# Optimization experiments

Measured on AMD Instinct MI355X. Metric: run time of the kernel, lower is better.

The kernel has to match this reference:

```python
import jax, jax.numpy as jnp
import numpy as np

N_NODES = 50000
N_EDGES = 600000
N_GRAPHS = 128
EMB = 128
LAYERS = 5
BN_EPS = 1e-5


def setup_inputs() -> dict:
    key = jax.random.key(0)
    ks = jax.random.split(key, 16)
    inp = {}
    inp['batch'] = jnp.sort(jax.random.randint(ks[0], (N_NODES,), 0, N_GRAPHS)).astype(jnp.int64 if jax.config.jax_enable_x64 else jnp.int32)
    inp['x'] = jax.random.normal(ks[1], (N_NODES, 48), dtype=jnp.float32)
    inp['edge_index'] = jax.random.randint(ks[2], (2, N_EDGES), 0, N_NODES)
    inp['edge_attr'] = jax.random.normal(ks[3], (N_EDGES, 11), dtype=jnp.float32)
    inp['edge_weight'] = jnp.ones((N_EDGES,), dtype=jnp.float32)
    # parameters (xavier-ish scaling)
    inp['W_atom'] = jax.random.normal(ks[4], (48, EMB), dtype=jnp.float32) * (1.0 / np.sqrt(48))
    inp['b_atom'] = jnp.zeros((EMB,), dtype=jnp.float32)
    inp['W_bond'] = jax.random.normal(ks[5], (11, EMB), dtype=jnp.float32) * (1.0 / np.sqrt(11))
    inp['b_bond'] = jnp.zeros((EMB,), dtype=jnp.float32)
    inp['Wl'] = jax.random.normal(ks[6], (LAYERS, EMB, EMB), dtype=jnp.float32) * (1.0 / np.sqrt(EMB))
    inp['bl'] = jnp.zeros((LAYERS, EMB), dtype=jnp.float32)
    inp['Wr'] = jax.random.normal(ks[7], (LAYERS, EMB, EMB), dtype=jnp.float32) * (1.0 / np.sqrt(EMB))
    inp['gamma'] = jnp.ones((LAYERS, EMB), dtype=jnp.float32)
    inp['beta'] = jnp.zeros((LAYERS, EMB), dtype=jnp.float32)
    return inp


def reference(batch, x, edge_index, edge_attr, edge_weight,
              W_atom, b_atom, W_bond, b_bond, Wl, bl, Wr, gamma, beta):
    src = edge_index[0]
    dst = edge_index[1]
    # encoders
    h = x @ W_atom + b_atom                      # [N, EMB]
    ea = edge_attr @ W_bond + b_bond             # [E, EMB]
    # mean-aggregation denominator (in-degree, count-based)
    deg = jax.ops.segment_sum(jnp.ones_like(edge_weight), dst, num_segments=N_NODES)
    denom = jnp.maximum(deg, 1.0)[:, None]       # [N, 1]
    xs = []
    for i in range(LAYERS):
        # SAGEConv: mean over (x_j + edge_attr) * w_e, then lin_l(agg) + lin_r(x)
        msg = (h[src] + ea) * edge_weight[:, None]          # [E, EMB]
        agg = jax.ops.segment_sum(msg, dst, num_segments=N_NODES) / denom
        h = agg @ Wl[i] + bl[i] + h @ Wr[i]
        # BatchNorm1d (training: batch statistics, biased variance)
        mu = jnp.mean(h, axis=0)
        var = jnp.var(h, axis=0)
        h = gamma[i] * (h - mu) * jax.lax.rsqrt(var + BN_EPS) + beta[i]
        if i < LAYERS - 1:
            h = jax.nn.relu(h)
        # dropout with drop_ratio=0.0 is identity
        xs.append(h)
    # layerwise global_add_pool + concat
    xpool = jnp.concatenate(
        [jax.ops.segment_sum(xi, batch, num_segments=N_GRAPHS) for xi in xs], axis=1)
    return (xpool, h)
```

## Files before the change

kernel.cpp:

```cpp
#include <hip/hip_runtime.h>
#include <hip/hip_bf16.h>

#define NNODES 50000
#define NEDGES 600000
#define NGRAPHS 128
#define EMB 128
#define NLAYERS 5
#define BN_EPS 1e-5f
#define STATW 8
#define SCAN_BLOCKS ((NNODES + 255) / 256)
#define NSB ((NNODES + 255) / 256)
#define EAB ((NNODES + 31) / 32)
#define BPB ((NLAYERS * 32768 + 255) / 256)

typedef short s16x8 __attribute__((ext_vector_type(8)));
typedef float f32x16 __attribute__((ext_vector_type(16)));

__device__ __forceinline__ short f2bf(float f) {
    unsigned u = __builtin_bit_cast(unsigned, f);
    unsigned r = (u + 0x7fffu + ((u >> 16) & 1u)) >> 16;
    return (short)r;
}
__device__ __forceinline__ float bf2f(short s) {
    return __builtin_bit_cast(float, ((unsigned)(unsigned short)s) << 16);
}

__device__ __forceinline__ float2 stat_sum(const float* __restrict__ st, int t) {
    float s = 0.f, q = 0.f;
#pragma unroll
    for (int k = 0; k < STATW; k++) {
        s += st[k * 256 + t];
        q += st[k * 256 + 128 + t];
    }
    return make_float2(s, q);
}

__global__ __launch_bounds__(256) void init_kernel(int* __restrict__ deg,
                                                   float* __restrict__ stat) {
    int i = blockIdx.x * 256 + threadIdx.x;
    if (i < NNODES) deg[i] = 0;
    if (i < NLAYERS * STATW * 256) stat[i] = 0.f;
}

__global__ __launch_bounds__(256) void deg_kernel(const int* __restrict__ ei,
                                                  int* __restrict__ deg,
                                                  int* __restrict__ rank) {
    int e = blockIdx.x * 256 + threadIdx.x;
    if (e >= NEDGES) return;
    rank[e] = atomicAdd(&deg[ei[NEDGES + e]], 1);
}

__global__ __launch_bounds__(256) void scan1(const int* __restrict__ deg,
                                             int* __restrict__ local_excl,
                                             int* __restrict__ part) {
    __shared__ int sh[256];
    int t = threadIdx.x;
    int i = blockIdx.x * 256 + t;
    int v = (i < NNODES) ? deg[i] : 0;
    sh[t] = v;
    __syncthreads();
    for (int off = 1; off < 256; off <<= 1) {
        int u = (t >= off) ? sh[t - off] : 0;
        __syncthreads();
        sh[t] += u;
        __syncthreads();
    }
    if (i < NNODES) local_excl[i] = sh[t] - v;
    if (t == 255) part[blockIdx.x] = sh[255];
}

__global__ __launch_bounds__(256) void scan23(const int* __restrict__ part,
                                              const int* __restrict__ local_excl,
                                              int* __restrict__ rowptr) {
    __shared__ int sh[256];
    int t = threadIdx.x;
    int v = (t < SCAN_BLOCKS) ? part[t] : 0;
    sh[t] = v;
    __syncthreads();
    for (int off = 1; off < 256; off <<= 1) {
        int u = (t >= off) ? sh[t - off] : 0;
        __syncthreads();
        sh[t] += u;
        __syncthreads();
    }
    int bo = (blockIdx.x == 0) ? 0 : sh[blockIdx.x - 1];
    int i = blockIdx.x * 256 + t;
    if (i < NNODES) rowptr[i] = local_excl[i] + bo;
    if (blockIdx.x == 0 && t == 0) rowptr[NNODES] = sh[SCAN_BLOCKS - 1];
}

__global__ __launch_bounds__(256) void edge_fill(const int* __restrict__ ei,
                                                 const float* __restrict__ ew,
                                                 const float* __restrict__ eattr,
                                                 const int* __restrict__ rowptr,
                                                 const int* __restrict__ rank,
                                                 int* __restrict__ epk) {
    int e = blockIdx.x * 256 + threadIdx.x;
    if (e >= NEDGES) return;
    int src = ei[e];
    int dst = ei[NEDGES + e];
    int pos = rowptr[dst] + rank[e];
    int pk[8];
    pk[0] = src;
    pk[1] = __float_as_int(ew[e]);
    unsigned short a[12];
#pragma unroll
    for (int j = 0; j < 11; j++) a[j] = (unsigned short)f2bf(eattr[e * 11 + j]);
    a[11] = 0;
#pragma unroll
    for (int j = 0; j < 6; j++)
        pk[2 + j] = (int)a[2 * j] | ((int)a[2 * j + 1] << 16);
    int* dstp = epk + (size_t)pos * 8;
    *(int4*)dstp = *(int4*)pk;
    *(int4*)(dstp + 4) = *(int4*)(pk + 4);
}

__global__ __launch_bounds__(256) void prep2(const int* __restrict__ rowptr,
                                             const int* __restrict__ epk,
                                             int2* __restrict__ epg,
                                             const float* __restrict__ Wb,
                                             const float* __restrict__ bbond,
                                             short* __restrict__ Ehi,
                                             const float* __restrict__ X,
                                             const float* __restrict__ Wa,
                                             const float* __restrict__ ba,
                                             short* __restrict__ Hhi,
                                             const float* __restrict__ Wl,
                                             const float* __restrict__ Wr,
                                             short* __restrict__ Bf) {
    __shared__ float shpool[1792];
    int blk = blockIdx.x;
    int t = threadIdx.x;

    if (blk < NSB) {
        float* Wb_s = shpool;
        float* bb_s = shpool + 1408;
        for (int i = t; i < 1408; i += 256) Wb_s[i] = Wb[i];
        if (t < 128) bb_s[t] = bbond[t];
        __syncthreads();
        int node = blk * 256 + t;
        if (node >= NNODES) return;
        int b = rowptr[node], e = rowptr[node + 1];
        float s[11];
#pragma unroll
        for (int j = 0; j < 11; j++) s[j] = 0.f;
        float ws = 0.f;
        for (int p = b; p < e; p++) {
            const int* pk = epk + (size_t)p * 8;
            int4 lo = *(const int4*)pk;
            int4 hi = *(const int4*)(pk + 4);
            float w = __int_as_float(lo.y);
            ws += w;
            epg[p] = make_int2(lo.x, lo.y);
            int packed[6] = {lo.z, lo.w, hi.x, hi.y, hi.z, hi.w};
#pragma unroll
            for (int j = 0; j < 11; j++) {
                short v = (short)((packed[j >> 1] >> ((j & 1) * 16)) & 0xffff);
                s[j] += bf2f(v) * w;
            }
        }
        short* erow = Ehi + (size_t)node * 128;
#pragma unroll
        for (int c8 = 0; c8 < 16; c8++) {
            s16x8 o;
#pragma unroll
            for (int jj = 0; jj < 8; jj++) {
                int c = c8 * 8 + jj;
                float a = bb_s[c] * ws;
#pragma unroll
                for (int j = 0; j < 11; j++) a += s[j] * Wb_s[j * 128 + c];
                o[jj] = f2bf(a);
            }
            *(s16x8*)(erow + c8 * 8) = o;
        }
    } else if (blk < NSB + EAB) {
        float* as = shpool;
        int row0 = (blk - NSB) * 32;
        for (int i = t; i < 32 * 48; i += 256) {
            int r = i / 48, k = i - r * 48;
            int gr = row0 + r;
            as[k * 36 + r] = (gr < NNODES) ? X[gr * 48 + k] : 0.f;
        }
        __syncthreads();
        int c = t & 127, rh = t >> 7;
        float acc[16];
#pragma unroll
        for (int i = 0; i < 16; i++) acc[i] = 0.f;
        for (int k = 0; k < 48; k++) {
            float w = Wa[k * 128 + c];
            const float* rowv = &as[k * 36 + rh * 16];
            float4 v0 = *(const float4*)(rowv + 0);
            float4 v1 = *(const float4*)(rowv + 4);
            float4 v2 = *(const float4*)(rowv + 8);
            float4 v3 = *(const float4*)(rowv + 12);
            acc[0] += v0.x * w;  acc[1] += v0.y * w;
            acc[2] += v0.z * w;  acc[3] += v0.w * w;
            acc[4] += v1.x * w;  acc[5] += v1.y * w;
            acc[6] += v1.z * w;  acc[7] += v1.w * w;
            acc[8] += v2.x * w;  acc[9] += v2.y * w;
            acc[10] += v2.z * w; acc[11] += v2.w * w;
            acc[12] += v3.x * w; acc[13] += v3.y * w;
            acc[14] += v3.z * w; acc[15] += v3.w * w;
        }
        float bb = ba[c];
        for (int i = 0; i < 16; i++) {
            int gr = row0 + rh * 16 + i;
            if (gr < NNODES) Hhi[(size_t)gr * 128 + c] = f2bf(acc[i] + bb);
        }
    } else {
        int idx = (blk - NSB - EAB) * 256 + t;
        if (idx >= NLAYERS * 32768) return;
        int layer = idx >> 15;
        int r = idx & 32767;
        int k = r >> 7, col = r & 127;
        float w = (k < 128) ? Wl[layer * 16384 + k * 128 + col]
                            : Wr[layer * 16384 + (k - 128) * 128 + col];
        short hi = f2bf(w);
        short lo = f2bf(w - bf2f(hi));
        int ks = k >> 4, half = (k >> 3) & 1, j = k & 7;
        int nt = col >> 5, n32 = col & 31;
        int fo = ((nt * 2 + half) * 32 + n32) * 8 + j;
        short* base = Bf + (size_t)layer * 65536 + ks * 4096;
        base[fo] = hi;
        base[2048 + fo] = lo;
    }
}

__global__ __launch_bounds__(256) void agg_kernel(const short* __restrict__ Hsrc,
                                                  const short* __restrict__ Ehi,
                                                  const int* __restrict__ rowptr,
                                                  const int2* __restrict__ epg,
                                                  const float* __restrict__ stat,
                                                  const float* __restrict__ gamma,
                                                  const float* __restrict__ beta,
                                                  short* __restrict__ Ahi) {
    __shared__ float cscs[128], cshs[128];
    int t = threadIdx.x;
    if (t < 128) {
        float sc = 1.f, sh = 0.f;
        if (stat) {
            const float invM = 1.f / (float)NNODES;
            float2 sq = stat_sum(stat, t);
            float mu = sq.x * invM;
            float var = sq.y * invM - mu * mu;
            sc = gamma[t] * rsqrtf(var + BN_EPS);
            sh = beta[t] - mu * sc;
        }
        cscs[t] = sc;
        cshs[t] = sh;
    }
    __syncthreads();
    int lane = t & 15, grp = t >> 4;
    int c8 = lane * 8;
    int node = blockIdx.x * 16 + grp;
    if (node >= NNODES) return;
    float rlo = stat ? 0.f : -3.4e38f;
    float sc[8], sh[8];
#pragma unroll
    for (int j = 0; j < 8; j++) { sc[j] = cscs[c8 + j]; sh[j] = cshs[c8 + j]; }
    int b = rowptr[node], e = rowptr[node + 1];
    float s[8];
#pragma unroll
    for (int j = 0; j < 8; j++) s[j] = 0.f;
    int p = b;
    for (; p + 3 < e; p += 4) {
        int2 e0 = epg[p], e1 = epg[p + 1], e2 = epg[p + 2], e3 = epg[p + 3];
        float w0 = __int_as_float(e0.y), w1 = __int_as_float(e1.y);
        float w2 = __int_as_float(e2.y), w3 = __int_as_float(e3.y);
        s16x8 h0 = *(const s16x8*)&Hsrc[(size_t)e0.x * 128 + c8];
        s16x8 h1 = *(const s16x8*)&Hsrc[(size_t)e1.x * 128 + c8];
        s16x8 h2 = *(const s16x8*)&Hsrc[(size_t)e2.x * 128 + c8];
        s16x8 h3 = *(const s16x8*)&Hsrc[(size_t)e3.x * 128 + c8];
#pragma unroll
        for (int j = 0; j < 8; j++) {
            float v0 = fmaxf(bf2f(h0[j]) * sc[j] + sh[j], rlo);
            float v1 = fmaxf(bf2f(h1[j]) * sc[j] + sh[j], rlo);
            float v2 = fmaxf(bf2f(h2[j]) * sc[j] + sh[j], rlo);
            float v3 = fmaxf(bf2f(h3[j]) * sc[j] + sh[j], rlo);
            s[j] += v0 * w0 + v1 * w1 + v2 * w2 + v3 * w3;
        }
    }
    for (; p < e; p++) {
        int2 pk0 = epg[p];
        float w0 = __int_as_float(pk0.y);
        s16x8 h0 = *(const s16x8*)&Hsrc[(size_t)pk0.x * 128 + c8];
#pragma unroll
        for (int j = 0; j < 8; j++)
            s[j] += fmaxf(bf2f(h0[j]) * sc[j] + sh[j], rlo) * w0;
    }
    float inv = 1.f / fmaxf((float)(e - b), 1.f);
    s16x8 ea = *(const s16x8*)&Ehi[(size_t)node * 128 + c8];
    s16x8 o;
#pragma unroll
    for (int j = 0; j < 8; j++) o[j] = f2bf((s[j] + bf2f(ea[j])) * inv);
    *(s16x8*)&Ahi[(size_t)node * 128 + c8] = o;
}

__global__ __launch_bounds__(256) void layer_gemm(const short* __restrict__ Ahi,
                                                  const short* __restrict__ Hsrc,
                                                  const float* __restrict__ statp,
                                                  const float* __restrict__ gamma,
                                                  const float* __restrict__ beta,
                                                  const short* __restrict__ Bf,
                                                  const float* __restrict__ bias,
                                                  short* __restrict__ Cbf,
                                                  float* __restrict__ stat) {
    __shared__ float s_s[128], s_q[128];
    __shared__ float csc[128], csh[128];
    int t = threadIdx.x;
    int wave = t >> 6, lane = t & 63;
    int n32 = lane & 31, half = lane >> 5;
    int row0 = blockIdx.x * 128 + wave * 32;

    if (t < 128) {
        s_s[t] = 0.f;
        s_q[t] = 0.f;
        float sc = 1.f, sh = 0.f;
        if (statp) {
            const float invM = 1.f / (float)NNODES;
            float2 sq = stat_sum(statp, t);
            float mu = sq.x * invM;
            float var = sq.y * invM - mu * mu;
            sc = gamma[t] * rsqrtf(var + BN_EPS);
            sh = beta[t] - mu * sc;
        }
        csc[t] = sc;
        csh[t] = sh;
    }
    __syncthreads();
    float rlo = statp ? 0.f : -3.4e38f;

    int myrow = row0 + n32;
    bool rowok = myrow < NNODES;
    size_t rbase = (size_t)myrow * 128;
    int acol = half * 8;

    f32x16 acc[4];
#pragma unroll
    for (int i = 0; i < 4; i++) acc[i] = (f32x16)(0.f);

    const short* bb0 = Bf + half * 256 + n32 * 8;

    s16x8 ahA = {0, 0, 0, 0, 0, 0, 0, 0}, ahB = {0, 0, 0, 0, 0, 0, 0, 0};
    s16x8 bhA[4], blA[4], bhB[4], blB[4];
    if (rowok) {
        ahA = *(const s16x8*)(Ahi + rbase + acol);
        ahB = *(const s16x8*)(Ahi + rbase + 16 + acol);
    }
#pragma unroll
    for (int nt = 0; nt < 4; nt++) {
        bhA[nt] = *(const s16x8*)(bb0 + nt * 512);
        blA[nt] = *(const s16x8*)(bb0 + 2048 + nt * 512);
        bhB[nt] = *(const s16x8*)(bb0 + 4096 + nt * 512);
        blB[nt] = *(const s16x8*)(bb0 + 4096 + 2048 + nt * 512);
    }

#pragma unroll
    for (int ks = 0; ks < 16; ks++) {
        s16x8 ahC = {0, 0, 0, 0, 0, 0, 0, 0};
        s16x8 bhC[4], blC[4];
        if (ks < 14) {
            int kn = ks + 2;
            if (rowok) {
                if (kn < 8) {
                    ahC = *(const s16x8*)(Ahi + rbase + kn * 16 + acol);
                } else {
                    s16x8 hv = *(const s16x8*)(Hsrc + rbase + (kn & 7) * 16 + acol);
                    int kc = (kn & 7) * 16 + acol;
#pragma unroll
                    for (int j = 0; j < 8; j++)
                        ahC[j] = f2bf(fmaxf(bf2f(hv[j]) * csc[kc + j] +
                                            csh[kc + j], rlo));
                }
            }
            const short* bbn = bb0 + kn * 4096;
#pragma unroll
            for (int nt = 0; nt < 4; nt++) {
                bhC[nt] = *(const s16x8*)(bbn + nt * 512);
                blC[nt] = *(const s16x8*)(bbn + 2048 + nt * 512);
            }
        }
#pragma unroll
        for (int nt = 0; nt < 4; nt++) {
            acc[nt] = __builtin_amdgcn_mfma_f32_32x32x16_bf16(ahA, bhA[nt], acc[nt], 0, 0, 0);
            acc[nt] = __builtin_amdgcn_mfma_f32_32x32x16_bf16(ahA, blA[nt], acc[nt], 0, 0, 0);
        }
        ahA = ahB;
        ahB = ahC;
#pragma unroll
        for (int nt = 0; nt < 4; nt++) {
            bhA[nt] = bhB[nt];
            blA[nt] = blB[nt];
            bhB[nt] = bhC[nt];
            blB[nt] = blC[nt];
        }
    }

#pragma unroll
    for (int nt = 0; nt < 4; nt++) {
        int col = nt * 32 + n32;
        float bb = bias[col];
        float ss = 0.f, qq = 0.f;
#pragma unroll
        for (int reg = 0; reg < 16; reg++) {
            int r = row0 + (reg & 3) + 8 * (reg >> 2) + 4 * half;
            if (r < NNODES) {
                float v = acc[nt][reg] + bb;
                Cbf[(size_t)r * 128 + col] = f2bf(v);
                ss += v;
                qq += v * v;
            }
        }
        ss += __shfl_xor(ss, 32);
        qq += __shfl_xor(qq, 32);
        if (half == 0) {
            atomicAdd(&s_s[col], ss);
            atomicAdd(&s_q[col], qq);
        }
    }
    __syncthreads();
    if (t < 128) {
        int slot = blockIdx.x & (STATW - 1);
        atomicAdd(&stat[slot * 256 + t], s_s[t]);
        atomicAdd(&stat[slot * 256 + 128 + t], s_q[t]);
    }
}

__global__ __launch_bounds__(256) void pool5(const short* __restrict__ Cbf,
                                             const float* __restrict__ stat,
                                             const float* __restrict__ gamma,
                                             const float* __restrict__ beta,
                                             const int* __restrict__ batch,
                                             float* __restrict__ pool,
                                             float* __restrict__ Hf32) {
    __shared__ float csc[128], csh[128];
    __shared__ float sred[8][128];
    __shared__ int srange[2];
    int t = threadIdx.x;
    int u = blockIdx.x;
    int g = u / NLAYERS, l = u - g * NLAYERS;
    if (t < 2) {
        int target = g + t;
        int lo = 0, hi = NNODES;
        while (lo < hi) {
            int mid = (lo + hi) >> 1;
            if (batch[mid] < target) lo = mid + 1; else hi = mid;
        }
        srange[t] = lo;
    }
    if (t < 128) {
        const float invM = 1.f / (float)NNODES;
        float2 sq = stat_sum(stat + l * STATW * 256, t);
        float mu = sq.x * invM;
        float var = sq.y * invM - mu * mu;
        float sc = gamma[l * 128 + t] * rsqrtf(var + BN_EPS);
        csc[t] = sc;
        csh[t] = beta[l * 128 + t] - mu * sc;
    }
    __syncthreads();
    int gstart = srange[0], gend = srange[1];
    int lane = t & 31, grp = t >> 5;
    int c4 = lane * 4;
    float4 sc = *(const float4*)&csc[c4];
    float4 sh = *(const float4*)&csh[c4];
    const short* Cl = Cbf + (size_t)l * NNODES * 128;
    float4 accp = make_float4(0.f, 0.f, 0.f, 0.f);
    int relu = (l < NLAYERS - 1);
    for (int r = gstart + grp; r < gend; r += 8) {
        ushort4 cv = *(const ushort4*)&Cl[(size_t)r * 128 + c4];
        float4 v;
        v.x = bf2f((short)cv.x) * sc.x + sh.x;
        v.y = bf2f((short)cv.y) * sc.y + sh.y;
        v.z = bf2f((short)cv.z) * sc.z + sh.z;
        v.w = bf2f((short)cv.w) * sc.w + sh.w;
        if (relu) {
            v.x = fmaxf(v.x, 0.f);
            v.y = fmaxf(v.y, 0.f);
            v.z = fmaxf(v.z, 0.f);
            v.w = fmaxf(v.w, 0.f);
        } else {
            *(float4*)&Hf32[(size_t)r * 128 + c4] = v;
        }
        accp.x += v.x;
        accp.y += v.y;
        accp.z += v.z;
        accp.w += v.w;
    }
    sred[grp][c4 + 0] = accp.x;
    sred[grp][c4 + 1] = accp.y;
    sred[grp][c4 + 2] = accp.z;
    sred[grp][c4 + 3] = accp.w;
    __syncthreads();
    if (t < 128) {
        float s = 0.f;
#pragma unroll
        for (int k = 0; k < 8; k++) s += sred[k][t];
        pool[(size_t)g * 640 + l * 128 + t] = s;
    }
}

extern "C" void kernel_launch(void* const* d_in, const int* in_sizes, int n_in,
                              void* d_out, int out_size, void* d_ws, size_t ws_size,
                              hipStream_t stream) {
    const int* batch = (const int*)d_in[0];
    const float* x = (const float*)d_in[1];
    const int* edge_index = (const int*)d_in[2];
    const float* edge_attr = (const float*)d_in[3];
    const float* edge_weight = (const float*)d_in[4];
    const float* W_atom = (const float*)d_in[5];
    const float* b_atom = (const float*)d_in[6];
    const float* W_bond = (const float*)d_in[7];
    const float* b_bond = (const float*)d_in[8];
    const float* Wl = (const float*)d_in[9];
    const float* bl = (const float*)d_in[10];
    const float* Wr = (const float*)d_in[11];
    const float* gamma = (const float*)d_in[12];
    const float* beta = (const float*)d_in[13];
    float* out = (float*)d_out;

    char* ws = (char*)d_ws;
    size_t off = 0;
    auto alloc = [&](size_t bytes) -> void* {
        void* p = ws + off;
        off += (bytes + 255) & ~(size_t)255;
        return p;
    };
    short* Hhi = (short*)alloc((size_t)NNODES * 128 * 2);
    short* Ahi = (short*)alloc((size_t)NNODES * 128 * 2);
    short* Ehi = (short*)alloc((size_t)NNODES * 128 * 2);
    short* Cbf = (short*)alloc((size_t)NLAYERS * NNODES * 128 * 2);
    int* epk = (int*)alloc((size_t)NEDGES * 32);
    int2* epg = (int2*)alloc((size_t)NEDGES * 8);
    int* rank = (int*)alloc((size_t)NEDGES * 4);
    int* rowptr = (int*)alloc((size_t)(NNODES + 1) * 4);
    int* deg = (int*)alloc((size_t)NNODES * 4);
    float* stat = (float*)alloc(NLAYERS * STATW * 256 * 4);
    int* local_excl = (int*)alloc((size_t)NNODES * 4);
    int* part = (int*)alloc(SCAN_BLOCKS * 4);
    short* Bf = (short*)alloc((size_t)NLAYERS * 65536 * 2);

    init_kernel<<<SCAN_BLOCKS, 256, 0, stream>>>(deg, stat);
    deg_kernel<<<(NEDGES + 255) / 256, 256, 0, stream>>>(edge_index, deg, rank);
    scan1<<<SCAN_BLOCKS, 256, 0, stream>>>(deg, local_excl, part);
    scan23<<<SCAN_BLOCKS, 256, 0, stream>>>(part, local_excl, rowptr);
    edge_fill<<<(NEDGES + 255) / 256, 256, 0, stream>>>(edge_index, edge_weight,
                                                        edge_attr, rowptr, rank, epk);
    prep2<<<NSB + EAB + BPB, 256, 0, stream>>>(rowptr, epk, epg, W_bond, b_bond, Ehi,
                                               x, W_atom, b_atom, Hhi, Wl, Wr, Bf);

    const short* src = Hhi;
    for (int i = 0; i < NLAYERS; i++) {
        const float* st = (i == 0) ? nullptr : stat + (size_t)(i - 1) * STATW * 256;
        const float* gm = (i == 0) ? nullptr : gamma + (i - 1) * 128;
        const float* bt = (i == 0) ? nullptr : beta + (i - 1) * 128;
        short* Ci = Cbf + (size_t)i * NNODES * 128;
        agg_kernel<<<(NNODES + 15) / 16, 256, 0, stream>>>(src, Ehi, rowptr, epg,
                                                           st, gm, bt, Ahi);
        layer_gemm<<<(NNODES + 127) / 128, 256, 0, stream>>>(
            Ahi, src, st, gm, bt, Bf + (size_t)i * 65536, bl + i * 128, Ci,
            stat + (size_t)i * STATW * 256);
        src = Ci;
    }

    pool5<<<NGRAPHS * NLAYERS, 256, 0, stream>>>(
        Cbf, stat, gamma, beta, batch, out, out + (size_t)NGRAPHS * 640);
}
```

Before: 491.2 us.

## Split edge-encoder nodes across 8 lanes and use MFMA for atom encoder

```diff
diff --git a/kernel.cpp b/kernel.cpp
--- a/kernel.cpp
+++ b/kernel.cpp
@@ -9,9 +9,9 @@
 #define BN_EPS 1e-5f
 #define STATW 8
 #define SCAN_BLOCKS ((NNODES + 255) / 256)
-#define NSB ((NNODES + 255) / 256)
-#define EAB ((NNODES + 31) / 32)
-#define BPB ((NLAYERS * 32768 + 255) / 256)
+#define NSB2 ((NNODES + 31) / 32)
+#define EAMB ((NNODES + 127) / 128)
+#define BPB2 ((NLAYERS * 32768 + 255) / 256)
 
 typedef short s16x8 __attribute__((ext_vector_type(8)));
 typedef float f32x16 __attribute__((ext_vector_type(16)));
@@ -36,10 +36,23 @@
 }
 
 __global__ __launch_bounds__(256) void init_kernel(int* __restrict__ deg,
-                                                   float* __restrict__ stat) {
+                                                   float* __restrict__ stat,
+                                                   const float* __restrict__ Wa,
+                                                   short* __restrict__ Waf) {
     int i = blockIdx.x * 256 + threadIdx.x;
     if (i < NNODES) deg[i] = 0;
     if (i < NLAYERS * STATW * 256) stat[i] = 0.f;
+    if (i < 48 * 128) {
+        int k = i >> 7, col = i & 127;
+        float w = Wa[k * 128 + col];
+        short hi = f2bf(w);
+        short lo = f2bf(w - bf2f(hi));
+        int ks = k >> 4, half = (k >> 3) & 1, j = k & 7;
+        int nt = col >> 5, n32 = col & 31;
+        int fo = ((nt * 2 + half) * 32 + n32) * 8 + j;
+        Waf[ks * 4096 + fo] = hi;
+        Waf[ks * 4096 + 2048 + fo] = lo;
+    }
 }
 
 __global__ __launch_bounds__(256) void deg_kernel(const int* __restrict__ ei,
@@ -122,93 +135,111 @@
                                              const float* __restrict__ bbond,
                                              short* __restrict__ Ehi,
                                              const float* __restrict__ X,
-                                             const float* __restrict__ Wa,
                                              const float* __restrict__ ba,
                                              short* __restrict__ Hhi,
                                              const float* __restrict__ Wl,
                                              const float* __restrict__ Wr,
-                                             short* __restrict__ Bf) {
-    __shared__ float shpool[1792];
+                                             short* __restrict__ Bf,
+                                             const short* __restrict__ Waf) {
+    __shared__ float shpool[1536];
     int blk = blockIdx.x;
     int t = threadIdx.x;
 
-    if (blk < NSB) {
+    if (blk < NSB2) {
         float* Wb_s = shpool;
         float* bb_s = shpool + 1408;
         for (int i = t; i < 1408; i += 256) Wb_s[i] = Wb[i];
         if (t < 128) bb_s[t] = bbond[t];
         __syncthreads();
-        int node = blk * 256 + t;
-        if (node >= NNODES) return;
-        int b = rowptr[node], e = rowptr[node + 1];
+        int sub = t & 7, slot = t >> 3;
+        int node = blk * 32 + slot;
         float s[11];
 #pragma unroll
         for (int j = 0; j < 11; j++) s[j] = 0.f;
         float ws = 0.f;
-        for (int p = b; p < e; p++) {
-            const int* pk = epk + (size_t)p * 8;
-            int4 lo = *(const int4*)pk;
-            int4 hi = *(const int4*)(pk + 4);
-            float w = __int_as_float(lo.y);
-            ws += w;
-            epg[p] = make_int2(lo.x, lo.y);
-            int packed[6] = {lo.z, lo.w, hi.x, hi.y, hi.z, hi.w};
-#pragma unroll
-            for (int j = 0; j < 11; j++) {
-                short v = (short)((packed[j >> 1] >> ((j & 1) * 16)) & 0xffff);
-                s[j] += bf2f(v) * w;
-            }
-        }
-        short* erow = Ehi + (size_t)node * 128;
-#pragma unroll
-        for (int c8 = 0; c8 < 16; c8++) {
-            s16x8 o;
-#pragma unroll
-            for (int jj = 0; jj < 8; jj++) {
-                int c = c8 * 8 + jj;
-                float a = bb_s[c] * ws;
-#pragma unroll
-                for (int j = 0; j < 11; j++) a += s[j] * Wb_s[j * 128 + c];
-                o[jj] = f2bf(a);
-            }
-            *(s16x8*)(erow + c8 * 8) = o;
-        }
-    } else if (blk < NSB + EAB) {
-        float* as = shpool;
-        int row0 = (blk - NSB) * 32;
-        for (int i = t; i < 32 * 48; i += 256) {
-            int r = i / 48, k = i - r * 48;
-            int gr = row0 + r;
-            as[k * 36 + r] = (gr < NNODES) ? X[gr * 48 + k] : 0.f;
-        }
-        __syncthreads();
-        int c = t & 127, rh = t >> 7;
-        float acc[16];
-#pragma unroll
-        for (int i = 0; i < 16; i++) acc[i] = 0.f;
-        for (int k = 0; k < 48; k++) {
-            float w = Wa[k * 128 + c];
-            const float* rowv = &as[k * 36 + rh * 16];
-            float4 v0 = *(const float4*)(rowv + 0);
-            float4 v1 = *(const float4*)(rowv + 4);
-            float4 v2 = *(const float4*)(rowv + 8);
-            float4 v3 = *(const float4*)(rowv + 12);
-            acc[0] += v0.x * w;  acc[1] += v0.y * w;
-            acc[2] += v0.z * w;  acc[3] += v0.w * w;
-            acc[4] += v1.x * w;  acc[5] += v1.y * w;
-            acc[6] += v1.z * w;  acc[7] += v1.w * w;
-            acc[8] += v2.x * w;  acc[9] += v2.y * w;
-            acc[10] += v2.z * w; acc[11] += v2.w * w;
-            acc[12] += v3.x * w; acc[13] += v3.y * w;
-            acc[14] += v3.z * w; acc[15] += v3.w * w;
-        }
-        float bb = ba[c];
-        for (int i = 0; i < 16; i++) {
-            int gr = row0 + rh * 16 + i;
-            if (gr < NNODES) Hhi[(size_t)gr * 128 + c] = f2bf(acc[i] + bb);
+        if (node < NNODES) {
+            int b = rowptr[node], e = rowptr[node + 1];
+            for (int p = b + sub; p < e; p += 8) {
+                const int* pk = epk + (size_t)p * 8;
+                int4 lo = *(const int4*)pk;
+                int4 hi = *(const int4*)(pk + 4);
+                float w = __int_as_float(lo.y);
+                ws += w;
+                epg[p] = make_int2(lo.x, lo.y);
+                int packed[6] = {lo.z, lo.w, hi.x, hi.y, hi.z, hi.w};
+#pragma unroll
+                for (int j = 0; j < 11; j++) {
+                    short v = (short)((packed[j >> 1] >> ((j & 1) * 16)) & 0xffff);
+                    s[j] += bf2f(v) * w;
+                }
+            }
+        }
+#pragma unroll
+        for (int m = 1; m < 8; m <<= 1) {
+#pragma unroll
+            for (int j = 0; j < 11; j++) s[j] += __shfl_xor(s[j], m);
+            ws += __shfl_xor(ws, m);
+        }
+        if (node < NNODES) {
+            int c0 = sub * 16;
+            short* erow = Ehi + (size_t)node * 128 + c0;
+#pragma unroll
+            for (int cc = 0; cc < 2; cc++) {
+                s16x8 o;
+#pragma unroll
+                for (int jj = 0; jj < 8; jj++) {
+                    int c = c0 + cc * 8 + jj;
+                    float a = bb_s[c] * ws;
+#pragma unroll
+                    for (int j = 0; j < 11; j++) a += s[j] * Wb_s[j * 128 + c];
+                    o[jj] = f2bf(a);
+                }
+                *(s16x8*)(erow + cc * 8) = o;
+            }
+        }
+    } else if (blk < NSB2 + EAMB) {
+        int wave = t >> 6, lane = t & 63;
+        int n32 = lane & 31, half = lane >> 5;
+        int row0 = (blk - NSB2) * 128 + wave * 32;
+        int myrow = row0 + n32;
+        bool rowok = myrow < NNODES;
+        f32x16 acc[4];
+#pragma unroll
+        for (int i = 0; i < 4; i++) acc[i] = (f32x16)(0.f);
+        const short* wb0 = Waf + half * 256 + n32 * 8;
+#pragma unroll
+        for (int ks = 0; ks < 3; ks++) {
+            s16x8 ah = {0, 0, 0, 0, 0, 0, 0, 0};
+            if (rowok) {
+                const float* xp = X + (size_t)myrow * 48 + ks * 16 + half * 8;
+                float4 x0 = *(const float4*)xp;
+                float4 x1 = *(const float4*)(xp + 4);
+                ah[0] = f2bf(x0.x); ah[1] = f2bf(x0.y);
+                ah[2] = f2bf(x0.z); ah[3] = f2bf(x0.w);
+                ah[4] = f2bf(x1.x); ah[5] = f2bf(x1.y);
+                ah[6] = f2bf(x1.z); ah[7] = f2bf(x1.w);
+            }
+            const short* wbn = wb0 + ks * 4096;
+#pragma unroll
+            for (int nt = 0; nt < 4; nt++) {
+                s16x8 bh = *(const s16x8*)(wbn + nt * 512);
+                s16x8 bl = *(const s16x8*)(wbn + 2048 + nt * 512);
+                acc[nt] = __builtin_amdgcn_mfma_f32_32x32x16_bf16(ah, bh, acc[nt], 0, 0, 0);
+                acc[nt] = __builtin_amdgcn_mfma_f32_32x32x16_bf16(ah, bl, acc[nt], 0, 0, 0);
+            }
+        }
+#pragma unroll
+        for (int nt = 0; nt < 4; nt++) {
+            int col = nt * 32 + n32;
+            float bb = ba[col];
+#pragma unroll
+            for (int reg = 0; reg < 16; reg++) {
+                int r = row0 + (reg & 3) + 8 * (reg >> 2) + 4 * half;
+                if (r < NNODES) Hhi[(size_t)r * 128 + col] = f2bf(acc[nt][reg] + bb);
+            }
         }
     } else {
-        int idx = (blk - NSB - EAB) * 256 + t;
+        int idx = (blk - NSB2 - EAMB) * 256 + t;
         if (idx >= NLAYERS * 32768) return;
         int layer = idx >> 15;
         int r = idx & 32767;
@@ -538,15 +569,17 @@
     int* local_excl = (int*)alloc((size_t)NNODES * 4);
     int* part = (int*)alloc(SCAN_BLOCKS * 4);
     short* Bf = (short*)alloc((size_t)NLAYERS * 65536 * 2);
-
-    init_kernel<<<SCAN_BLOCKS, 256, 0, stream>>>(deg, stat);
+    short* Waf = (short*)alloc((size_t)3 * 4096 * 2);
+
+    init_kernel<<<SCAN_BLOCKS, 256, 0, stream>>>(deg, stat, W_atom, Waf);
     deg_kernel<<<(NEDGES + 255) / 256, 256, 0, stream>>>(edge_index, deg, rank);
     scan1<<<SCAN_BLOCKS, 256, 0, stream>>>(deg, local_excl, part);
     scan23<<<SCAN_BLOCKS, 256, 0, stream>>>(part, local_excl, rowptr);
     edge_fill<<<(NEDGES + 255) / 256, 256, 0, stream>>>(edge_index, edge_weight,
                                                         edge_attr, rowptr, rank, epk);
-    prep2<<<NSB + EAB + BPB, 256, 0, stream>>>(rowptr, epk, epg, W_bond, b_bond, Ehi,
-                                               x, W_atom, b_atom, Hhi, Wl, Wr, Bf);
+    prep2<<<NSB2 + EAMB + BPB2, 256, 0, stream>>>(rowptr, epk, epg, W_bond, b_bond,
+                                                  Ehi, x, b_atom, Hhi,
+                                                  Wl, Wr, Bf, Waf);
 
     const short* src = Hhi;
     for (int i = 0; i < NLAYERS; i++) {
```

New measurement: 482.3 us (median of 2 runs). About the same (-1.8%).
